# Optimization experiments

Measured on AMD Instinct MI355X. Metric: run time of the kernel, lower is better.

The kernel has to match this reference:

```python
import jax, jax.numpy as jnp
import numpy as np

NUM_HEADS = 12


def _attend(q, k, v, scale):
    # q: [B,H,Q,D], k/v: [B,H,K,D]
    attn = jnp.einsum('bhqd,bhkd->bhqk', q, k) * scale
    attn = jax.nn.softmax(attn, axis=-1)
    return jnp.einsum('bhqk,bhkd->bhqd', attn, v)


def setup_inputs() -> dict:
    key = jax.random.key(0)
    k1, k2, k3 = jax.random.split(key, 3)
    B, N, C = 32, 1009, 768
    x = jax.random.normal(k1, (B, N, C), dtype=jnp.float32)
    W_qkv = jax.random.normal(k2, (C, 3 * C), dtype=jnp.float32) * (C ** -0.5)
    b_qkv = jnp.zeros((3 * C,), dtype=jnp.float32)
    W_proj = jax.random.normal(k3, (C, C), dtype=jnp.float32) * (C ** -0.5)
    b_proj = jnp.zeros((C,), dtype=jnp.float32)
    return {"x": x, "W_qkv": W_qkv, "b_qkv": b_qkv, "W_proj": W_proj,
            "b_proj": b_proj, "query_len": 1, "lens_z": 432}


def reference(x, W_qkv, b_qkv, W_proj, b_proj, query_len, lens_z):
    B, N, C = x.shape
    H = NUM_HEADS
    D = C // H
    scale = D ** -0.5
    lens_x = N - query_len - lens_z

    qkv = (x @ W_qkv + b_qkv).reshape(B, N, 3, H, D)
    qkv = jnp.transpose(qkv, (2, 0, 3, 1, 4))  # [3,B,H,N,D]
    q, k, v = qkv[0], qkv[1], qkv[2]

    sl_p = slice(0, query_len)
    sl_t = slice(query_len, query_len + lens_z)
    sl_s = slice(query_len + lens_z, N)

    # prompt: local self-attention
    x_prompt = _attend(q[:, :, sl_p], k[:, :, sl_p], v[:, :, sl_p], scale)
    # template: local self-attention
    x_template = _attend(q[:, :, sl_t], k[:, :, sl_t], v[:, :, sl_t], scale)
    # search: global attention over all tokens
    x_search = _attend(q[:, :, sl_s], k, v, scale)

    def merge(y, L):
        return jnp.transpose(y, (0, 2, 1, 3)).reshape(B, L, C)

    out = jnp.concatenate([merge(x_prompt, query_len),
                           merge(x_template, lens_z),
                           merge(x_search, lens_x)], axis=1)
    return out @ W_proj + b_proj
```

## Files before the change

### kernel.cpp

```cpp
#include <hip/hip_runtime.h>

#define B_ 32
#define N_ 1009
#define C_ 768
#define H_ 12
#define D_ 64
#define M_ (B_*N_)
#define MT_ 253
#define MPAD_ (MT_*128)
#define NKV_ 1024

typedef __attribute__((ext_vector_type(4))) float f32x4;
typedef __attribute__((ext_vector_type(8))) short s16x8;

__device__ __forceinline__ unsigned short f2bf(float f) {
  union { float f; unsigned u; } x; x.f = f;
  unsigned r = x.u + 0x7fffu + ((x.u >> 16) & 1u);
  return (unsigned short)(r >> 16);
}

__device__ __forceinline__ f32x4 mfma16(s16x8 a, s16x8 b, f32x4 c) {
  return __builtin_amdgcn_mfma_f32_16x16x32_bf16(a, b, c, 0, 0, 0);
}

__device__ __forceinline__ void async16(const void* g, void* l) {
  __builtin_amdgcn_global_load_lds((const __attribute__((address_space(1))) void*)g,
                                   (__attribute__((address_space(3))) void*)l, 16, 0, 0);
}

__device__ __forceinline__ float exp2_fast(float x) {
  float r; asm("v_exp_f32 %0, %1" : "=v"(r) : "v"(x)); return r;
}

__device__ __forceinline__ unsigned cvt_pk_bf16(float lo, float hi) {
  unsigned r; asm("v_cvt_pk_bf16_f32 %0, %1, %2" : "=v"(r) : "v"(lo), "v"(hi)); return r;
}

template<int NWG>
__device__ __forceinline__ int xcd_swz(int bid) {
  constexpr int q = NWG >> 3, r = NWG & 7;
  const int x = bid & 7, l = bid >> 3;
  return (x < r ? x * (q + 1) : r * (q + 1) + (x - r) * q) + l;
}

__global__ void convert_x(const float* __restrict__ x, unsigned short* __restrict__ xb) {
  const long e = ((long)blockIdx.x * 256 + threadIdx.x) * 8;
  const long row = e / 768;
  s16x8 v;
  if (row < M_) {
#pragma unroll
    for (int j = 0; j < 8; ++j) v[j] = (short)f2bf(x[e + j]);
  } else {
    v = (s16x8){0,0,0,0,0,0,0,0};
  }
  *(s16x8*)&xb[e] = v;
}

__global__ void transpose_convert(const float* __restrict__ in, unsigned short* __restrict__ out,
                                  int R, int Ccols) {
  __shared__ float tile[64][65];
  const int tc = blockIdx.x * 64, tr = blockIdx.y * 64;
#pragma unroll
  for (int i = 0; i < 16; ++i) {
    const int e = i * 256 + threadIdx.x;
    const int r = e >> 6, c = e & 63;
    tile[r][c] = in[(long)(tr + r) * Ccols + tc + c];
  }
  __syncthreads();
#pragma unroll
  for (int i = 0; i < 16; ++i) {
    const int e = i * 256 + threadIdx.x;
    const int c = e >> 6, r = e & 63;
    out[(long)(tc + c) * R + tr + r] = f2bf(tile[r][c]);
  }
}

__global__ void zero_pad(unsigned short* __restrict__ kb, unsigned short* __restrict__ vt) {
  const int t = blockIdx.x * 256 + threadIdx.x;
  if (t >= 368640) return;
  const int d = t & 63;
  const int r = t >> 6;
  const int bh = r / 15, tok = 1009 + (r - bh * 15);
  kb[(((long)bh << 10) + tok) * 64 + d] = 0;
  const int c = t % 15, row = t / 15;
  vt[((long)row << 10) + 1009 + c] = 0;
}

template<int MODE>
__global__ __launch_bounds__(256, 2)
void gemm_bt(const unsigned short* __restrict__ A,
             const unsigned short* __restrict__ Bt,
             const float* __restrict__ bias,
             unsigned short* __restrict__ qo,
             unsigned short* __restrict__ ko,
             unsigned short* __restrict__ vo,
             float* __restrict__ fo) {
  __shared__ __align__(16) unsigned short smem[128 * 136];
  unsigned short* const As = smem;
  unsigned short* const Bs = smem + 4096;
  const int tid = threadIdx.x;
  const int lane = tid & 63;
  const int wv = tid >> 6;
  constexpr int NBN = (MODE == 0) ? 18 : 6;
  const int swzid = xcd_swz<MT_ * NBN>(blockIdx.x);
  const int bm = swzid / NBN;
  const int bn = swzid - bm * NBN;
  const int row0 = bm * 128;
  const int col0 = bn * 128;
  const int wr = (wv >> 1) * 64;
  const int wc = (wv & 1) * 64;

  f32x4 acc[4][4] = {};
  for (int kt = 0; kt < 768; kt += 32) {
#pragma unroll
    for (int c = 0; c < 2; ++c) {
      const int lds_byte = c * 4096 + wv * 1024;
      const int gg = c * 256 + wv * 64 + lane;
      const int row = gg >> 2;
      const int ck = ((gg & 3) ^ ((row >> 1) & 3)) << 3;
      async16(A + (long)(row0 + row) * 768 + kt + ck, (char*)As + lds_byte);
      async16(Bt + (long)(col0 + row) * 768 + kt + ck, (char*)Bs + lds_byte);
    }
    __syncthreads();
    s16x8 af[4], bfr[4];
#pragma unroll
    for (int m = 0; m < 4; ++m) {
      const int rA = wr + m * 16 + (lane & 15);
      af[m] = *(const s16x8*)&As[rA * 32 + (((lane >> 4) ^ ((rA >> 1) & 3)) << 3)];
    }
#pragma unroll
    for (int n = 0; n < 4; ++n) {
      const int rB = wc + n * 16 + (lane & 15);
      bfr[n] = *(const s16x8*)&Bs[rB * 32 + (((lane >> 4) ^ ((rB >> 1) & 3)) << 3)];
    }
#pragma unroll
    for (int m = 0; m < 4; ++m)
#pragma unroll
      for (int n = 0; n < 4; ++n)
        acc[m][n] = mfma16(af[m], bfr[n], acc[m][n]);
    __syncthreads();
  }

  if (MODE == 0 && col0 >= 1536) {
#pragma unroll
    for (int m = 0; m < 4; ++m)
#pragma unroll
      for (int j = 0; j < 4; ++j)
#pragma unroll
        for (int n = 0; n < 4; ++n) {
          const int dl = wc + n * 16 + (lane & 15);
          const int tk = wr + m * 16 + (lane >> 4) * 4 + j;
          smem[dl * 136 + tk] = f2bf(acc[m][n][j] + bias[col0 + dl]);
        }
    __syncthreads();
    const int h0 = (col0 - 1536) >> 6;
    const int b0 = row0 / N_;
    const int split = (b0 + 1) * N_ - row0;
#pragma unroll
    for (int it = 0; it < 8; ++it) {
      const int g = it * 256 + tid;
      const int dl = g >> 4;
      const int t8 = (g & 15) * 8;
      const s16x8 vv = *(const s16x8*)&smem[dl * 136 + t8];
      const int hh = h0 + (dl >> 6), dd = dl & 63;
#pragma unroll
      for (int jj = 0; jj < 8; ++jj) {
        const int tkb = t8 + jj;
        const int grow = row0 + tkb;
        if (grow < M_) {
          const int bb = (tkb < split) ? b0 : b0 + 1;
          const int ntok = grow - bb * N_;
          vo[(((((long)bb * H_ + hh) << 6) + dd) << 10) + ntok] = (unsigned short)vv[jj];
        }
      }
    }
    return;
  }

#pragma unroll
  for (int m = 0; m < 4; ++m) {
#pragma unroll
    for (int j = 0; j < 4; ++j) {
      const int grow = row0 + wr + m * 16 + (lane >> 4) * 4 + j;
      if (grow < M_) {
        if (MODE == 0) {
          const int b = grow / N_;
          const int ntok = grow - b * N_;
#pragma unroll
          for (int n = 0; n < 4; ++n) {
            const int col = col0 + wc + n * 16 + (lane & 15);
            float val = acc[m][n][j] + bias[col];
            const int which = col >= 768;
            if (!which) val *= 0.18033688011112042f;
            const int rem = col - which * 768;
            const int h = rem >> 6, d = rem & 63;
            const long bh = (long)b * H_ + h;
            unsigned short* dst = which ? ko : qo;
            dst[((bh << 10) + ntok) * 64 + d] = f2bf(val);
          }
        } else {
#pragma unroll
          for (int n = 0; n < 4; ++n) {
            const int col = col0 + wc + n * 16 + (lane & 15);
            fo[(long)grow * 768 + col] = acc[m][n][j] + bias[col];
          }
        }
      }
    }
  }
}

__global__ void misc_copy(const unsigned short* __restrict__ vt, unsigned short* __restrict__ og) {
  const int t = blockIdx.x * 256 + threadIdx.x;
  if (t >= B_ * H_ * D_) return;
  const int d = t & 63;
  const int bh = t >> 6;
  const int b = bh / H_, h = bh - b * H_;
  og[((long)b * N_) * 768 + h * 64 + d] = vt[(((long)bh << 6) + d) << 10];
}

__global__ __launch_bounds__(256, 4)
void attn_kernel(const unsigned short* __restrict__ qg,
                 const unsigned short* __restrict__ kg,
                 const unsigned short* __restrict__ vtg,
                 unsigned short* __restrict__ og) {
  __shared__ __align__(16) unsigned short Ks[2][64 * 64];
  __shared__ __align__(16) unsigned short Vts[2][64 * 64];
  __shared__ __align__(16) unsigned short Ps[64 * 64];

  const int bid = blockIdx.x;
  const int swz = (bid & 7) * 768 + (bid >> 3);
  const int tile = swz & 15;
  const int bh = swz >> 4;
  const int b = bh / H_;
  const int h = bh - b * H_;
  int qbase, qend, kstart, ktiles, kend;
  if (tile < 7) { qbase = 1 + 64 * tile;       qend = 433;  kstart = 1; ktiles = 7;  kend = 433; }
  else          { qbase = 433 + 64 * (tile-7); qend = 1009; kstart = 0; ktiles = 16; kend = 1009; }
  const long base  = (long)bh << 10;
  const long vbase = (long)bh << 6;
  const int tid = threadIdx.x, lane = tid & 63, wv = tid >> 6;
  const int q15 = lane & 15, q7 = lane & 7, g = lane >> 4;

  s16x8 qa[2];
  {
    const unsigned short* qp = qg + (base + qbase + wv * 16 + q15) * 64;
    qa[0] = *(const s16x8*)(qp + g * 8);
    qa[1] = *(const s16x8*)(qp + 32 + g * 8);
  }
  asm volatile("s_waitcnt vmcnt(0)" ::: "memory");

  f32x4 o[4] = {};
  float mrow = -1e30f, lrow = 0.f;

  auto stage = [&](int bufsel, int kb0) {
#pragma unroll
    for (int it = 0; it < 2; ++it) {
      const int ldsoff = (it * 256 + wv * 64) * 16;
      const int gr = it * 256 + wv * 64 + lane;
      const int rl = gr >> 3;
      const int cs = (gr & 7) ^ (rl & 7);
      async16(kg + ((base + kb0 + rl) << 6) + cs * 8, (char*)&Ks[bufsel][0] + ldsoff);
      async16(vtg + ((vbase + rl) << 10) + kb0 + cs * 8, (char*)&Vts[bufsel][0] + ldsoff);
    }
  };

  const int prow = wv * 16 + q15;

  stage(0, kstart);
  for (int kt = 0; kt < ktiles; ++kt) {
    const int buf = kt & 1;
    const int kbase0 = kstart + 64 * kt;
    if (kt + 1 < ktiles) {
      stage(buf ^ 1, kbase0 + 64);
      asm volatile("s_waitcnt vmcnt(4)" ::: "memory");
    } else {
      asm volatile("s_waitcnt vmcnt(0)" ::: "memory");
    }
    __builtin_amdgcn_s_barrier();

    f32x4 s4[4];
    __builtin_amdgcn_s_setprio(1);
#pragma unroll
    for (int n = 0; n < 4; ++n) {
      const int krow = n * 16 + q15;
      const int r7 = krow & 7;
      f32x4 a = {};
      a = mfma16(*(const s16x8*)&Ks[buf][krow * 64 + ((g ^ r7) << 3)],       qa[0], a);
      a = mfma16(*(const s16x8*)&Ks[buf][krow * 64 + (((4 + g) ^ r7) << 3)], qa[1], a);
      s4[n] = a;
    }
    __builtin_amdgcn_s_setprio(0);

    if (kbase0 + 64 > kend) {
#pragma unroll
      for (int n = 0; n < 4; ++n)
#pragma unroll
        for (int j = 0; j < 4; ++j)
          if (kbase0 + n * 16 + g * 4 + j >= kend) s4[n][j] = -1e30f;
    }

    float rmax = fmaxf(
        fmaxf(fmaxf(fmaxf(s4[0][0], s4[0][1]), fmaxf(s4[0][2], s4[0][3])),
              fmaxf(fmaxf(s4[1][0], s4[1][1]), fmaxf(s4[1][2], s4[1][3]))),
        fmaxf(fmaxf(fmaxf(s4[2][0], s4[2][1]), fmaxf(s4[2][2], s4[2][3])),
              fmaxf(fmaxf(s4[3][0], s4[3][1]), fmaxf(s4[3][2], s4[3][3]))));
    rmax = fmaxf(rmax, __shfl_xor(rmax, 16));
    rmax = fmaxf(rmax, __shfl_xor(rmax, 32));

    const float mnew = fmaxf(mrow, rmax);
    const float corr = exp2_fast(mrow - mnew);
    mrow = mnew;
#pragma unroll
    for (int f = 0; f < 4; ++f)
#pragma unroll
      for (int j = 0; j < 4; ++j) o[f][j] *= corr;

    float psum = 0.f;
#pragma unroll
    for (int n = 0; n < 4; ++n) {
#pragma unroll
      for (int j = 0; j < 4; ++j) {
        s4[n][j] = exp2_fast(s4[n][j] - mnew);
        psum += s4[n][j];
      }
      uint2 pw;
      pw.x = cvt_pk_bf16(s4[n][0], s4[n][1]);
      pw.y = cvt_pk_bf16(s4[n][2], s4[n][3]);
      *(uint2*)((char*)Ps + prow * 128 + (((n * 2 + (g >> 1)) ^ q7) << 4) + (g & 1) * 8) = pw;
    }
    psum += __shfl_xor(psum, 16);
    psum += __shfl_xor(psum, 32);
    lrow = lrow * corr + psum;

    s16x8 pa[2];
#pragma unroll
    for (int kf = 0; kf < 2; ++kf)
      pa[kf] = *(const s16x8*)((char*)Ps + prow * 128 + (((kf * 4 + g) ^ q7) << 4));
    __builtin_amdgcn_s_setprio(1);
#pragma unroll
    for (int f = 0; f < 4; ++f) {
      const int vrow = f * 16 + q15;
      const int v7 = vrow & 7;
#pragma unroll
      for (int kf = 0; kf < 2; ++kf) {
        const s16x8 vb = *(const s16x8*)&Vts[buf][vrow * 64 + (((kf * 4 + g) ^ v7) << 3)];
        o[f] = mfma16(vb, pa[kf], o[f]);
      }
    }
    __builtin_amdgcn_s_setprio(0);

    asm volatile("s_waitcnt lgkmcnt(0)" ::: "memory");
    __builtin_amdgcn_s_barrier();
  }

  const int qrow = qbase + wv * 16 + q15;
  if (qrow < qend) {
    const float inv = 1.0f / lrow;
    unsigned short* op = og + ((long)b * N_ + qrow) * 768 + h * 64 + g * 4;
#pragma unroll
    for (int f = 0; f < 4; ++f) {
      uint2 ow;
      ow.x = cvt_pk_bf16(o[f][0] * inv, o[f][1] * inv);
      ow.y = cvt_pk_bf16(o[f][2] * inv, o[f][3] * inv);
      *(uint2*)(op + f * 16) = ow;
    }
  }
}

extern "C" void kernel_launch(void* const* d_in, const int* in_sizes, int n_in,
                              void* d_out, int out_size, void* d_ws, size_t ws_size,
                              hipStream_t stream) {
  const float* x      = (const float*)d_in[0];
  const float* W_qkv  = (const float*)d_in[1];
  const float* b_qkv  = (const float*)d_in[2];
  const float* W_proj = (const float*)d_in[3];
  const float* b_proj = (const float*)d_in[4];
  float* out = (float*)d_out;

  unsigned short* ws = (unsigned short*)d_ws;
  unsigned short* wqkvT  = ws;
  unsigned short* wprojT = wqkvT + (long)2304 * 768;
  unsigned short* qb = wprojT + (long)768 * 768;
  const long kvsz = (long)B_ * H_ * NKV_ * D_;
  unsigned short* kb = qb + kvsz;
  unsigned short* vb = kb + kvsz;
  unsigned short* xb = vb + kvsz;
  unsigned short* attnout = xb;

  zero_pad<<<1440, 256, 0, stream>>>(kb, vb);
  convert_x<<<12144, 256, 0, stream>>>(x, xb);
  transpose_convert<<<dim3(2304 / 64, 768 / 64), 256, 0, stream>>>(W_qkv, wqkvT, 768, 2304);
  transpose_convert<<<dim3(768 / 64, 768 / 64), 256, 0, stream>>>(W_proj, wprojT, 768, 768);
  gemm_bt<0><<<MT_ * 18, 256, 0, stream>>>(xb, wqkvT, b_qkv, qb, kb, vb, nullptr);
  misc_copy<<<96, 256, 0, stream>>>(vb, attnout);
  attn_kernel<<<B_ * H_ * 16, 256, 0, stream>>>(qb, kb, vb, attnout);
  gemm_bt<1><<<MT_ * 6, 256, 0, stream>>>(attnout, wprojT, b_proj, nullptr, nullptr, nullptr, out);
}
```

Measured before the change: 418.5 us.

## Double-buffer GEMM LDS tiles with async prefetch and raise occupancy target

Splits the GEMM's shared-memory staging into two buffers, so the async global-to-LDS load of the next K-slice is issued before the current slice is computed. Explicit vmcnt waits and raw barriers replace the full __syncthreads. It also raises the launch-bounds occupancy hint to 4 blocks per CU and raises wave priority around the MFMA block. The aim is to hide global load latency behind matrix math, at the cost of tighter register limits that could cause spills.

```diff
diff --git a/kernel.cpp b/kernel.cpp
--- a/kernel.cpp
+++ b/kernel.cpp
@@ -87,7 +87,7 @@
 }
 
 template<int MODE>
-__global__ __launch_bounds__(256, 2)
+__global__ __launch_bounds__(256, 4)
 void gemm_bt(const unsigned short* __restrict__ A,
              const unsigned short* __restrict__ Bt,
              const float* __restrict__ bias,
@@ -95,9 +95,7 @@
              unsigned short* __restrict__ ko,
              unsigned short* __restrict__ vo,
              float* __restrict__ fo) {
-  __shared__ __align__(16) unsigned short smem[128 * 136];
-  unsigned short* const As = smem;
-  unsigned short* const Bs = smem + 4096;
+  __shared__ __align__(16) unsigned short smem[17408];
   const int tid = threadIdx.x;
   const int lane = tid & 63;
   const int wv = tid >> 6;
@@ -110,35 +108,53 @@
   const int wr = (wv >> 1) * 64;
   const int wc = (wv & 1) * 64;
 
-  f32x4 acc[4][4] = {};
-  for (int kt = 0; kt < 768; kt += 32) {
+  auto stage = [&](int bufsel, int kt) {
 #pragma unroll
     for (int c = 0; c < 2; ++c) {
-      const int lds_byte = c * 4096 + wv * 1024;
+      const int lds_off = c * 4096 + wv * 1024;
       const int gg = c * 256 + wv * 64 + lane;
       const int row = gg >> 2;
       const int ck = ((gg & 3) ^ ((row >> 1) & 3)) << 3;
-      async16(A + (long)(row0 + row) * 768 + kt + ck, (char*)As + lds_byte);
-      async16(Bt + (long)(col0 + row) * 768 + kt + ck, (char*)Bs + lds_byte);
-    }
-    __syncthreads();
+      async16(A + (long)(row0 + row) * 768 + kt + ck, (char*)smem + bufsel * 8192 + lds_off);
+      async16(Bt + (long)(col0 + row) * 768 + kt + ck, (char*)smem + 16384 + bufsel * 8192 + lds_off);
+    }
+  };
+
+  f32x4 acc[4][4] = {};
+  stage(0, 0);
+  for (int it = 0; it < 24; ++it) {
+    const int buf = it & 1;
+    if (it + 1 < 24) {
+      stage(buf ^ 1, (it + 1) * 32);
+      asm volatile("s_waitcnt vmcnt(4)" ::: "memory");
+    } else {
+      asm volatile("s_waitcnt vmcnt(0)" ::: "memory");
+    }
+    __builtin_amdgcn_s_barrier();
+
+    const unsigned short* Asb = smem + buf * 4096;
+    const unsigned short* Bsb = smem + 8192 + buf * 4096;
     s16x8 af[4], bfr[4];
 #pragma unroll
     for (int m = 0; m < 4; ++m) {
       const int rA = wr + m * 16 + (lane & 15);
-      af[m] = *(const s16x8*)&As[rA * 32 + (((lane >> 4) ^ ((rA >> 1) & 3)) << 3)];
+      af[m] = *(const s16x8*)&Asb[rA * 32 + (((lane >> 4) ^ ((rA >> 1) & 3)) << 3)];
     }
 #pragma unroll
     for (int n = 0; n < 4; ++n) {
       const int rB = wc + n * 16 + (lane & 15);
-      bfr[n] = *(const s16x8*)&Bs[rB * 32 + (((lane >> 4) ^ ((rB >> 1) & 3)) << 3)];
-    }
+      bfr[n] = *(const s16x8*)&Bsb[rB * 32 + (((lane >> 4) ^ ((rB >> 1) & 3)) << 3)];
+    }
+    __builtin_amdgcn_s_setprio(1);
 #pragma unroll
     for (int m = 0; m < 4; ++m)
 #pragma unroll
       for (int n = 0; n < 4; ++n)
         acc[m][n] = mfma16(af[m], bfr[n], acc[m][n]);
-    __syncthreads();
+    __builtin_amdgcn_s_setprio(0);
+
+    asm volatile("s_waitcnt lgkmcnt(0)" ::: "memory");
+    __builtin_amdgcn_s_barrier();
   }
 
   if (MODE == 0 && col0 >= 1536) {
```

Result: no change. 413.9 us (-1.1%).
